# Optimization experiments

Hardware: AMD Instinct MI355X
Metric: run time of the kernel (lower is better)

Reference implementation:

```python
import jax, jax.numpy as jnp
import numpy as np

INV_SQRT2 = 0.7071067811865476
INV_SQRT3 = 0.5773502691896258

N_ATOMS, N_EDGES = 5000, 50000
K3, K4 = 16, 16
N_TRIP, N_QUAD = N_EDGES * K3, N_EDGES * K4
N_INTERM = N_QUAD // 2
NSPH3, NSPH4 = 7, 16
E_ATOM, E_EDGE = 128, 512
E_TRIP, E_QUAD = 64, 64
E_RBF, E_CBF, E_SBF = 16, 16, 32
E_BIL_T, E_BIL_Q = 64, 32


def _w(key, shape):
    # He-style init, fan_in = second-to-last dim
    return jax.random.normal(key, shape, jnp.float32) / np.float32(np.sqrt(shape[-2]))


def setup_inputs() -> dict:
    ks = iter(jax.random.split(jax.random.key(0), 64))
    nk = lambda: next(ks)
    inp = {}
    inp['h'] = jax.random.normal(nk(), (N_ATOMS, E_ATOM), jnp.float32)
    inp['m'] = jax.random.normal(nk(), (N_EDGES, E_EDGE), jnp.float32)
    inp['rbf4'] = jax.random.normal(nk(), (N_EDGES, E_RBF), jnp.float32)
    inp['cbf4'] = jax.random.normal(nk(), (N_INTERM, E_CBF), jnp.float32)
    inp['rbf_W1_4'] = jax.random.normal(nk(), (N_EDGES, E_SBF, NSPH4), jnp.float32) * 0.1
    inp['sph4'] = jax.random.normal(nk(), (N_EDGES, K4, NSPH4), jnp.float32) * 0.1
    inp['rbf3'] = jax.random.normal(nk(), (N_EDGES, E_RBF), jnp.float32)
    inp['rbf_W1_3'] = jax.random.normal(nk(), (N_EDGES, E_CBF, NSPH3), jnp.float32) * 0.1
    inp['sph3'] = jax.random.normal(nk(), (N_EDGES, K3, NSPH3), jnp.float32) * 0.1
    inp['rbf_h'] = jax.random.normal(nk(), (N_EDGES, E_RBF), jnp.float32)
    # learned parameters
    inp['W_dense_ca'] = _w(nk(), (E_EDGE, E_EDGE))
    inp['Wq_db'] = _w(nk(), (E_EDGE, E_EDGE))
    inp['Wq_rbf'] = _w(nk(), (E_RBF, E_EDGE))
    inp['Wq_cbf'] = _w(nk(), (E_CBF, E_QUAD))
    inp['Wq_bil'] = jax.random.normal(nk(), (E_QUAD, E_SBF, E_BIL_Q), jnp.float32) / np.float32(np.sqrt(E_QUAD * E_SBF))
    inp['Wq_down'] = _w(nk(), (E_EDGE, E_QUAD))
    inp['Wq_up_ca'] = _w(nk(), (E_BIL_Q, E_EDGE))
    inp['Wq_up_ac'] = _w(nk(), (E_BIL_Q, E_EDGE))
    inp['Wt_ba'] = _w(nk(), (E_EDGE, E_EDGE))
    inp['Wt_rbf'] = _w(nk(), (E_RBF, E_EDGE))
    inp['Wt_bil'] = jax.random.normal(nk(), (E_TRIP, E_CBF, E_BIL_T), jnp.float32) / np.float32(np.sqrt(E_TRIP * E_CBF))
    inp['Wt_down'] = _w(nk(), (E_EDGE, E_TRIP))
    inp['Wt_up_ca'] = _w(nk(), (E_BIL_T, E_EDGE))
    inp['Wt_up_ac'] = _w(nk(), (E_BIL_T, E_EDGE))
    inp['W_before'] = _w(nk(), (1, 2, E_EDGE, E_EDGE))
    inp['W_after'] = _w(nk(), (2, 2, E_EDGE, E_EDGE))
    inp['W_au_rbf'] = _w(nk(), (E_RBF, E_EDGE))
    inp['W_au_dense'] = _w(nk(), (E_EDGE, E_ATOM))
    inp['W_au_res'] = _w(nk(), (3, 2, E_ATOM, E_ATOM))
    inp['W_concat'] = _w(nk(), (2 * E_ATOM + E_EDGE, E_EDGE))
    inp['W_resm'] = _w(nk(), (1, 2, E_EDGE, E_EDGE))
    # index tensors; (id_reduce, Kidx) pairs are collision-free by construction
    i32 = jnp.int32
    inp['Kidx4'] = jnp.tile(jnp.arange(K4, dtype=i32), N_EDGES)
    inp['id_swap'] = jax.random.permutation(nk(), N_EDGES).astype(i32)
    inp['id4_reduce_ca'] = jnp.repeat(jnp.arange(N_EDGES, dtype=i32), K4)
    inp['id4_expand_intm_db'] = jax.random.randint(nk(), (N_INTERM,), 0, N_EDGES, i32)
    inp['id4_expand_abd'] = jax.random.randint(nk(), (N_QUAD,), 0, N_INTERM, i32)
    inp['Kidx3'] = jnp.tile(jnp.arange(K3, dtype=i32), N_EDGES)
    inp['id3_expand_ba'] = jax.random.randint(nk(), (N_TRIP,), 0, N_EDGES, i32)
    inp['id3_reduce_ca'] = jnp.repeat(jnp.arange(N_EDGES, dtype=i32), K3)
    inp['idx_s'] = jax.random.randint(nk(), (N_EDGES,), 0, N_ATOMS, i32)
    inp['idx_t'] = jax.random.randint(nk(), (N_EDGES,), 0, N_ATOMS, i32)
    return inp


def _residual_stack(x, Ws):
    # Ws: (L, 2, U, U); GemNet ResidualLayer: (x + f(f(x))) / sqrt(2)
    for i in range(Ws.shape[0]):
        y = jax.nn.silu(jax.nn.silu(x @ Ws[i, 0]) @ Ws[i, 1])
        x = (x + y) * INV_SQRT2
    return x


def _bilinear(rbf_W1, sph, mvals, W, id_reduce, Kidx):
    # EfficientInteractionBilinear: scatter interactions into (nEdges, Kmax, emb),
    # contract with spherical basis, down-projected radial basis and bilinear weight.
    nE, Kmax = sph.shape[0], sph.shape[1]
    m2 = jnp.zeros((nE, Kmax, mvals.shape[-1]), mvals.dtype).at[id_reduce, Kidx].set(mvals)
    sum_k = jnp.einsum('ekn,ekh->enh', sph, m2)    # (nEdges, nSph, emb)
    r = jnp.einsum('ein,enh->eih', rbf_W1, sum_k)  # (nEdges, interm, emb)
    return jnp.einsum('eih,hiu->eu', r, W)         # (nEdges, units_out)


def reference(h, m, rbf4, cbf4, rbf_W1_4, sph4, rbf3, rbf_W1_3, sph3, rbf_h,
              W_dense_ca, Wq_db, Wq_rbf, Wq_cbf, Wq_bil, Wq_down, Wq_up_ca, Wq_up_ac,
              Wt_ba, Wt_rbf, Wt_bil, Wt_down, Wt_up_ca, Wt_up_ac,
              W_before, W_after, W_au_rbf, W_au_dense, W_au_res, W_concat, W_resm,
              Kidx4, id_swap, id4_reduce_ca, id4_expand_intm_db, id4_expand_abd,
              Kidx3, id3_expand_ba, id3_reduce_ca, idx_s, idx_t):
    silu = jax.nn.silu
    x_ca_skip = silu(m @ W_dense_ca)
    # ---- quadruplet interaction ----
    xq = silu(m @ Wq_db)
    xq = xq * (rbf4 @ Wq_rbf)        # Hadamard with RBF (ScalingFactor scale=1)
    xq = silu(xq @ Wq_down)          # (nEdges, E_QUAD)
    xq = xq[id4_expand_intm_db]      # (nInterm, E_QUAD)
    xq = xq * (cbf4 @ Wq_cbf)        # Hadamard with CBF
    xq = xq[id4_expand_abd]          # (nQuad, E_QUAD)
    xq = _bilinear(rbf_W1_4, sph4, xq, Wq_bil, id4_reduce_ca, Kidx4)
    x4 = (silu(xq @ Wq_up_ca) + silu(xq @ Wq_up_ac)[id_swap]) * INV_SQRT2
    # ---- triplet interaction ----
    xt = silu(m @ Wt_ba)
    xt = xt * (rbf3 @ Wt_rbf)
    xt = silu(xt @ Wt_down)          # (nEdges, E_TRIP)
    xt = xt[id3_expand_ba]           # (nTrip, E_TRIP)
    xt = _bilinear(rbf_W1_3, sph3, xt, Wt_bil, id3_reduce_ca, Kidx3)
    x3 = (silu(xt @ Wt_up_ca) + silu(xt @ Wt_up_ac)[id_swap]) * INV_SQRT2
    # ---- merge + residual stacks ----
    x = (x_ca_skip + x3 + x4) * INV_SQRT3
    x = _residual_stack(x, W_before)
    m = (m + x) * INV_SQRT2
    m = _residual_stack(m, W_after)
    # ---- atom update ----
    xa = m * (rbf_h @ W_au_rbf)
    xa = jax.ops.segment_sum(xa, idx_t, num_segments=h.shape[0])
    xa = silu(xa @ W_au_dense)
    xa = _residual_stack(xa, W_au_res)
    h = (h + xa) * INV_SQRT2
    # ---- concat / edge re-embedding ----
    m2 = jnp.concatenate([h[idx_s], h[idx_t], m], axis=-1)
    m2 = silu(m2 @ W_concat)
    m2 = _residual_stack(m2, W_resm)
    m = (m + m2) * INV_SQRT2
    return h, m
```

## Files before the change

### kernel.cpp

```cpp
#include <hip/hip_runtime.h>

#define INV_SQRT2f 0.70710678118654752440f
#define INV_SQRT3f 0.57735026918962576451f

typedef __bf16 bf16x8 __attribute__((ext_vector_type(8)));
typedef float f32x4 __attribute__((ext_vector_type(4)));

__device__ __forceinline__ float silu_f(float x) { return x / (1.0f + __expf(-x)); }

enum { EPI_SILU = 0, EPI_SILU_MUL = 1, EPI_ACC = 2, EPI_RES = 3, EPI_RES2 = 4, EPI_NONE = 5 };

struct WT { const float* src; __bf16* dst; int K; int N; };
struct WTBatch { WT d[18]; };

__global__ __launch_bounds__(256) void wconv_k(WTBatch b)
{
  __shared__ float t[64][65];
  const WT w = b.d[blockIdx.z];
  const int k0 = blockIdx.x << 6, n0 = blockIdx.y << 6;
  if (k0 >= w.K || n0 >= w.N) return;
  const int tx = threadIdx.x & 63, ty = threadIdx.x >> 6;
#pragma unroll
  for (int i = 0; i < 16; ++i) {
    const int k = (i << 2) + ty;
    const int gk = k0 + k, gn = n0 + tx;
    t[k][tx] = (gk < w.K && gn < w.N) ? w.src[(size_t)gk * w.N + gn] : 0.0f;
  }
  __syncthreads();
#pragma unroll
  for (int i = 0; i < 16; ++i) {
    const int n = (i << 2) + ty;
    const int gn = n0 + n, gk = k0 + tx;
    if (gn < w.N && gk < w.K) w.dst[(size_t)gn * w.K + gk] = (__bf16)t[tx][n];
  }
}

template <int EPI, bool CONCAT, bool ABF16 = false>
__global__ __launch_bounds__(256) void gemm_k(
    const float* A, const __bf16* W, float* C, int M, int N, int K,
    const float* mul, const int* perm, const float* res0, const float* res1,
    float scale, const float* h_src, const int* gidx_s, const int* gidx_t,
    const float* m_src)
{
  constexpr int LSTR = 40;
  __shared__ __bf16 As[128 * LSTR];
  __shared__ __bf16 Bs[128 * LSTR];
  const int tid  = threadIdx.x;
  const int lane = tid & 63;
  const int wave = tid >> 6;
  const int bm = blockIdx.x << 7;
  const int bn = blockIdx.y << 7;
  const int wm = (wave & 1) << 6;
  const int wn = (wave >> 1) << 6;
  const int fm = lane & 15;
  const int qk = (lane >> 4) << 3;

  f32x4 acc[4][4] = {};

  const int nkt = K >> 5;
  for (int kt = 0; kt < nkt; ++kt) {
    const int k0 = kt << 5;
    if constexpr (ABF16) {
      const __bf16* Ab = (const __bf16*)A;
#pragma unroll
      for (int i = 0; i < 2; ++i) {
        const int f   = tid + (i << 8);
        const int row = f >> 2;
        const int c8  = (f & 3) << 3;
        int gm = bm + row;
        if (gm >= M) gm = M - 1;
        const bf16x8 v = *(const bf16x8*)(Ab + (size_t)gm * K + k0 + c8);
        *(bf16x8*)&As[row * LSTR + c8] = v;
      }
    } else {
#pragma unroll
      for (int i = 0; i < 4; ++i) {
        const int f   = tid + (i << 8);
        const int row = f >> 3;
        const int c4  = (f & 7) << 2;
        int gm = bm + row;
        if (gm >= M) gm = M - 1;
        const int gk = k0 + c4;
        float4 v;
        if (CONCAT) {
          const float* src;
          if (gk < 128)      src = h_src + ((size_t)gidx_s[gm] << 7) + gk;
          else if (gk < 256) src = h_src + ((size_t)gidx_t[gm] << 7) + (gk - 128);
          else               src = m_src + ((size_t)gm << 9) + (gk - 256);
          v = *(const float4*)src;
        } else {
          v = *(const float4*)(A + (size_t)gm * K + gk);
        }
        __bf16* dst = &As[row * LSTR + c4];
        dst[0] = (__bf16)v.x; dst[1] = (__bf16)v.y;
        dst[2] = (__bf16)v.z; dst[3] = (__bf16)v.w;
      }
    }
#pragma unroll
    for (int i = 0; i < 2; ++i) {
      const int f  = tid + (i << 8);
      const int n  = f >> 2;
      const int c8 = (f & 3) << 3;
      int gn = bn + n;
      if (gn >= N) gn = N - 1;
      const bf16x8 v = *(const bf16x8*)(W + (size_t)gn * K + k0 + c8);
      *(bf16x8*)&Bs[n * LSTR + c8] = v;
    }
    __syncthreads();
    bf16x8 af[4], bfv[4];
#pragma unroll
    for (int mt = 0; mt < 4; ++mt)
      af[mt] = *(const bf16x8*)&As[(wm + mt * 16 + fm) * LSTR + qk];
#pragma unroll
    for (int nt = 0; nt < 4; ++nt)
      bfv[nt] = *(const bf16x8*)&Bs[(wn + nt * 16 + fm) * LSTR + qk];
#pragma unroll
    for (int mt = 0; mt < 4; ++mt)
#pragma unroll
      for (int nt = 0; nt < 4; ++nt)
        acc[mt][nt] = __builtin_amdgcn_mfma_f32_16x16x32_bf16(af[mt], bfv[nt], acc[mt][nt], 0, 0, 0);
    __syncthreads();
  }

#pragma unroll
  for (int mt = 0; mt < 4; ++mt) {
#pragma unroll
    for (int nt = 0; nt < 4; ++nt) {
#pragma unroll
      for (int r = 0; r < 4; ++r) {
        const int row = bm + wm + mt * 16 + ((lane >> 4) << 2) + r;
        const int col = bn + wn + nt * 16 + fm;
        if (row < M && col < N) {
          const float s = acc[mt][nt][r];
          const size_t o = (size_t)row * N + col;
          if constexpr (EPI == EPI_SILU) {
            C[o] = silu_f(s) * scale;
          } else if constexpr (EPI == EPI_SILU_MUL) {
            C[o] = silu_f(s) * mul[o];
          } else if constexpr (EPI == EPI_ACC) {
            const int rr = perm ? perm[row] : row;
            C[(size_t)rr * N + col] += silu_f(s) * scale;
          } else if constexpr (EPI == EPI_RES) {
            C[o] = (res0[o] + silu_f(s)) * scale;
          } else if constexpr (EPI == EPI_RES2) {
            C[o] = (res0[o] + (res1[o] + silu_f(s)) * INV_SQRT2f) * INV_SQRT2f;
          } else {
            C[o] = s * scale;
          }
        }
      }
    }
  }
}

__global__ __launch_bounds__(256) void rbf_proj_k(
    const float* __restrict__ rbf, const float* __restrict__ W,
    float* __restrict__ out, int M)
{
  const int g = blockIdx.x * 256 + threadIdx.x;
  const int e = g >> 9, c = g & 511;
  if (e >= M) return;
  const float* r = rbf + (size_t)e * 16;
  float s = 0.0f;
#pragma unroll
  for (int j = 0; j < 16; ++j) s += r[j] * W[(j << 9) + c];
  out[g] = s;
}

__global__ __launch_bounds__(256) void quad_interm_k(
    const float* __restrict__ xqe, const float* __restrict__ cbf,
    const float* __restrict__ Wcbf, const int* __restrict__ idb,
    float* __restrict__ out)
{
  __shared__ float Ws[1024];
  const int t = threadIdx.x;
  for (int i = t; i < 1024; i += 256) Ws[i] = Wcbf[i];
  __syncthreads();
  const int i = blockIdx.x * 4 + (t >> 6);
  const int c = t & 63;
  const float* cb = cbf + (size_t)i * 16;
  float s = 0.0f;
#pragma unroll
  for (int j = 0; j < 16; ++j) s += cb[j] * Ws[j * 64 + c];
  out[(size_t)i * 64 + c] = xqe[(size_t)idb[i] * 64 + c] * s;
}

__global__ __launch_bounds__(256) void quad_r_k(
    const float* __restrict__ BI, const float* __restrict__ sph,
    const float* __restrict__ rbfW, const int* __restrict__ abd,
    __bf16* __restrict__ R)
{
  __shared__ float sp[4][256];
  __shared__ float rw[4][512];
  const int t = threadIdx.x;
  const int lane = t & 63;
  const int w = t >> 6;
  const int e = blockIdx.x * 4 + w;

  *(float4*)&sp[w][lane << 2] = *(const float4*)(sph + (size_t)e * 256 + (lane << 2));
  *(float4*)&rw[w][lane << 2] = *(const float4*)(rbfW + (size_t)e * 512 + (lane << 2));
  *(float4*)&rw[w][256 + (lane << 2)] = *(const float4*)(rbfW + (size_t)e * 512 + 256 + (lane << 2));

  float val[16];
#pragma unroll
  for (int k = 0; k < 16; ++k)
    val[k] = BI[(size_t)abd[e * 16 + k] * 64 + lane];

  __syncthreads();

  float sumk[16] = {};
#pragma unroll
  for (int k = 0; k < 16; ++k) {
    const float v = val[k];
#pragma unroll
    for (int n = 0; n < 16; ++n) sumk[n] += sp[w][k * 16 + n] * v;
  }

#pragma unroll
  for (int ib = 0; ib < 4; ++ib) {
    bf16x8 pack;
#pragma unroll
    for (int j = 0; j < 8; ++j) {
      const int i = ib * 8 + j;
      float s = 0.0f;
#pragma unroll
      for (int n = 0; n < 16; ++n) s += rw[w][i * 16 + n] * sumk[n];
      pack[j] = (__bf16)s;
    }
    *(bf16x8*)(R + (size_t)e * 2048 + (lane << 5) + (ib << 3)) = pack;
  }
}

__global__ __launch_bounds__(256) void trip_r_k(
    const float* __restrict__ XTE, const float* __restrict__ sph,
    const float* __restrict__ rbfW, const int* __restrict__ ba,
    __bf16* __restrict__ R)
{
  __shared__ float sp[4][112];
  __shared__ float rw[4][112];
  const int t = threadIdx.x;
  const int lane = t & 63;
  const int w = t >> 6;
  const int e = blockIdx.x * 4 + w;

  if (lane < 28) {
    *(float4*)&sp[w][lane << 2] = *(const float4*)(sph + (size_t)e * 112 + (lane << 2));
  } else if (lane >= 32 && lane < 60) {
    const int q = (lane - 32) << 2;
    *(float4*)&rw[w][q] = *(const float4*)(rbfW + (size_t)e * 112 + q);
  }

  float val[16];
#pragma unroll
  for (int k = 0; k < 16; ++k)
    val[k] = XTE[(size_t)ba[e * 16 + k] * 64 + lane];

  __syncthreads();

  float sumk[7] = {};
#pragma unroll
  for (int k = 0; k < 16; ++k) {
    const float v = val[k];
#pragma unroll
    for (int n = 0; n < 7; ++n) sumk[n] += sp[w][k * 7 + n] * v;
  }

#pragma unroll
  for (int ib = 0; ib < 2; ++ib) {
    bf16x8 pack;
#pragma unroll
    for (int j = 0; j < 8; ++j) {
      const int i = ib * 8 + j;
      float s = 0.0f;
#pragma unroll
      for (int n = 0; n < 7; ++n) s += rw[w][i * 7 + n] * sumk[n];
      pack[j] = (__bf16)s;
    }
    *(bf16x8*)(R + (size_t)e * 1024 + (lane << 4) + (ib << 3)) = pack;
  }
}

__global__ __launch_bounds__(256) void inv_perm_k(const int* __restrict__ p,
                                                  int* __restrict__ inv, int n)
{
  const int i = blockIdx.x * 256 + threadIdx.x;
  if (i < n) inv[p[i]] = i;
}

__global__ __launch_bounds__(256) void zero_k(float* __restrict__ p, int n)
{
  const int i = blockIdx.x * 256 + threadIdx.x;
  if (i < n) p[i] = 0.0f;
}

__global__ __launch_bounds__(256) void atom_scatter_k(
    const float* __restrict__ mafter, const float* __restrict__ rh,
    const int* __restrict__ idxt, float* __restrict__ A0, int nE)
{
  const int g = blockIdx.x * 256 + threadIdx.x;
  const int e = g >> 9, c = g & 511;
  if (e >= nE) return;
  const size_t o = (size_t)e * 512 + c;
  atomicAdd(&A0[(size_t)idxt[e] * 512 + c], mafter[o] * rh[o]);
}

__global__ __launch_bounds__(256) void hout_k(const float* __restrict__ h,
                                              const float* __restrict__ xa,
                                              float* __restrict__ out, int n)
{
  const int i = blockIdx.x * 256 + threadIdx.x;
  if (i < n) out[i] = (h[i] + xa[i]) * INV_SQRT2f;
}

extern "C" void kernel_launch(void* const* d_in, const int* in_sizes, int n_in,
                              void* d_out, int out_size, void* d_ws, size_t ws_size,
                              hipStream_t stream) {
  (void)in_sizes; (void)n_in; (void)out_size; (void)ws_size;
  const float* h        = (const float*)d_in[0];
  const float* m        = (const float*)d_in[1];
  const float* rbf4     = (const float*)d_in[2];
  const float* cbf4     = (const float*)d_in[3];
  const float* rbfW4    = (const float*)d_in[4];
  const float* sph4     = (const float*)d_in[5];
  const float* rbf3     = (const float*)d_in[6];
  const float* rbfW3    = (const float*)d_in[7];
  const float* sph3     = (const float*)d_in[8];
  const float* rbf_h    = (const float*)d_in[9];
  const float* W_dense  = (const float*)d_in[10];
  const float* Wq_db    = (const float*)d_in[11];
  const float* Wq_rbf   = (const float*)d_in[12];
  const float* Wq_cbf   = (const float*)d_in[13];
  const float* Wq_bil   = (const float*)d_in[14];
  const float* Wq_down  = (const float*)d_in[15];
  const float* Wq_up_ca = (const float*)d_in[16];
  const float* Wq_up_ac = (const float*)d_in[17];
  const float* Wt_ba    = (const float*)d_in[18];
  const float* Wt_rbf   = (const float*)d_in[19];
  const float* Wt_bil   = (const float*)d_in[20];
  const float* Wt_down  = (const float*)d_in[21];
  const float* Wt_up_ca = (const float*)d_in[22];
  const float* Wt_up_ac = (const float*)d_in[23];
  const float* W_before = (const float*)d_in[24];
  const float* W_after  = (const float*)d_in[25];
  const float* W_au_rbf = (const float*)d_in[26];
  const float* W_au_dns = (const float*)d_in[27];
  const float* W_au_res = (const float*)d_in[28];
  const float* W_concat = (const float*)d_in[29];
  const float* W_resm   = (const float*)d_in[30];
  const int* id_swap    = (const int*)d_in[32];
  const int* id4_db     = (const int*)d_in[34];
  const int* id4_abd    = (const int*)d_in[35];
  const int* id3_ba     = (const int*)d_in[37];
  const int* idx_s      = (const int*)d_in[39];
  const int* idx_t      = (const int*)d_in[40];

  float* w = (float*)d_ws;
  const size_t S = 25600000;
  float* B0  = w;
  float* B1  = w + S;
  float* XQE = B1;
  float* XTE = B1;
  __bf16* RQ = (__bf16*)w;
  __bf16* RT = (__bf16*)w;
  float* R   = w + 2 * S;
  float* XQB = R;
  float* XTB = R + 1600000;
  float* A0  = R;
  float* A1  = R + 2560000;
  float* A2  = R + 3200000;
  int*   INV = (int*)(R + 4800000);

  float* out_h = (float*)d_out;
  float* out_m = out_h + 640000;
  float* BI    = out_m;

  WTBatch b1{}, b2{}, b3{};
  int n1 = 0, n2 = 0, n3 = 0;
  __bf16* z1p = (__bf16*)out_h;
  __bf16* z5p = (__bf16*)(R + 3840000);
  __bf16* z3p = (__bf16*)R;
  auto cv1 = [&](const float* s, int K, int N) { __bf16* d = z1p; z1p += (size_t)K * N; b1.d[n1++] = WT{s, d, K, N}; return d; };
  auto cv2 = [&](const float* s, int K, int N) { __bf16* d = z5p; z5p += (size_t)K * N; b2.d[n2++] = WT{s, d, K, N}; return d; };
  auto cv3 = [&](const float* s, int K, int N) { __bf16* d = z3p; z3p += (size_t)K * N; b3.d[n3++] = WT{s, d, K, N}; return d; };

  __bf16* Wb_q_db    = cv1(Wq_db,    512, 512);
  __bf16* Wb_q_down  = cv1(Wq_down,  512,  64);
  __bf16* Wb_q_bil   = cv1(Wq_bil,  2048,  32);
  __bf16* Wb_t_ba    = cv1(Wt_ba,    512, 512);
  __bf16* Wb_t_down  = cv1(Wt_down,  512,  64);
  __bf16* Wb_t_bil   = cv1(Wt_bil,  1024,  64);
  __bf16* Wb_dense   = cv1(W_dense,  512, 512);
  __bf16* Wb_q_up_ca = cv1(Wq_up_ca,  32, 512);
  __bf16* Wb_q_up_ac = cv1(Wq_up_ac,  32, 512);
  __bf16* Wb_t_up_ca = cv1(Wt_up_ca,  64, 512);
  __bf16* Wb_t_up_ac = cv1(Wt_up_ac,  64, 512);
  __bf16* Wb_au_dns  = cv1(W_au_dns, 512, 128);
  __bf16* Wb_au_res[6];
  for (int l = 0; l < 6; ++l) Wb_au_res[l] = cv1(W_au_res + (size_t)l * 16384, 128, 128);
  __bf16* Wb_before0 = cv2(W_before,          512, 512);
  __bf16* Wb_before1 = cv2(W_before + 262144, 512, 512);
  __bf16* Wb_after[4];
  for (int l = 0; l < 4; ++l) Wb_after[l] = cv2(W_after + (size_t)l * 262144, 512, 512);
  __bf16* Wb_concat  = cv3(W_concat,        768, 512);
  __bf16* Wb_resm0   = cv3(W_resm,          512, 512);
  __bf16* Wb_resm1   = cv3(W_resm + 262144, 512, 512);

  const float s23 = INV_SQRT2f * INV_SQRT3f;
  const dim3 blk(256);
  const dim3 gFull(391, 4), gN64(391, 1), gBil(391, 1), gAtom(40, 1);
#define NUL9 nullptr, nullptr, nullptr, nullptr
#define TAIL4 nullptr, nullptr, nullptr, nullptr

  wconv_k<<<dim3(32, 8, n1), blk, 0, stream>>>(b1);
  inv_perm_k<<<196, blk, 0, stream>>>(id_swap, INV, 50000);

  rbf_proj_k<<<100000, blk, 0, stream>>>(rbf4, Wq_rbf, B1, 50000);
  gemm_k<EPI_SILU_MUL, false><<<gFull, blk, 0, stream>>>(m, Wb_q_db, B0, 50000, 512, 512,
      B1, nullptr, nullptr, nullptr, 1.0f, TAIL4);
  gemm_k<EPI_SILU, false><<<gN64, blk, 0, stream>>>(B0, Wb_q_down, XQE, 50000, 64, 512,
      NUL9, 1.0f, TAIL4);
  quad_interm_k<<<100000, blk, 0, stream>>>(XQE, cbf4, Wq_cbf, id4_db, BI);
  quad_r_k<<<12500, blk, 0, stream>>>(BI, sph4, rbfW4, id4_abd, RQ);
  gemm_k<EPI_NONE, false, true><<<gBil, blk, 0, stream>>>((const float*)RQ, Wb_q_bil, XQB,
      50000, 32, 2048, NUL9, 1.0f, TAIL4);

  rbf_proj_k<<<100000, blk, 0, stream>>>(rbf3, Wt_rbf, B1, 50000);
  gemm_k<EPI_SILU_MUL, false><<<gFull, blk, 0, stream>>>(m, Wb_t_ba, B0, 50000, 512, 512,
      B1, nullptr, nullptr, nullptr, 1.0f, TAIL4);
  gemm_k<EPI_SILU, false><<<gN64, blk, 0, stream>>>(B0, Wb_t_down, XTE, 50000, 64, 512,
      NUL9, 1.0f, TAIL4);
  trip_r_k<<<12500, blk, 0, stream>>>(XTE, sph3, rbfW3, id3_ba, RT);
  gemm_k<EPI_NONE, false, true><<<gBil, blk, 0, stream>>>((const float*)RT, Wb_t_bil, XTB,
      50000, 64, 1024, NUL9, 1.0f, TAIL4);

  gemm_k<EPI_SILU, false><<<gFull, blk, 0, stream>>>(m, Wb_dense, B0, 50000, 512, 512,
      NUL9, INV_SQRT3f, TAIL4);
  gemm_k<EPI_ACC, false><<<gFull, blk, 0, stream>>>(XQB, Wb_q_up_ca, B0, 50000, 512, 32,
      nullptr, nullptr, nullptr, nullptr, s23, TAIL4);
  gemm_k<EPI_ACC, false><<<gFull, blk, 0, stream>>>(XQB, Wb_q_up_ac, B0, 50000, 512, 32,
      nullptr, INV, nullptr, nullptr, s23, TAIL4);
  gemm_k<EPI_ACC, false><<<gFull, blk, 0, stream>>>(XTB, Wb_t_up_ca, B0, 50000, 512, 64,
      nullptr, nullptr, nullptr, nullptr, s23, TAIL4);
  gemm_k<EPI_ACC, false><<<gFull, blk, 0, stream>>>(XTB, Wb_t_up_ac, B0, 50000, 512, 64,
      nullptr, INV, nullptr, nullptr, s23, TAIL4);

  wconv_k<<<dim3(8, 8, n2), blk, 0, stream>>>(b2);

  gemm_k<EPI_SILU, false><<<gFull, blk, 0, stream>>>(B0, Wb_before0, B1, 50000, 512, 512,
      NUL9, 1.0f, TAIL4);
  gemm_k<EPI_RES2, false><<<gFull, blk, 0, stream>>>(B1, Wb_before1, out_m, 50000, 512, 512,
      nullptr, nullptr, m, B0, 1.0f, TAIL4);
  gemm_k<EPI_SILU, false><<<gFull, blk, 0, stream>>>(out_m, Wb_after[0], B1, 50000, 512, 512,
      NUL9, 1.0f, TAIL4);
  gemm_k<EPI_RES, false><<<gFull, blk, 0, stream>>>(B1, Wb_after[1], out_m, 50000, 512, 512,
      nullptr, nullptr, out_m, nullptr, INV_SQRT2f, TAIL4);
  gemm_k<EPI_SILU, false><<<gFull, blk, 0, stream>>>(out_m, Wb_after[2], B1, 50000, 512, 512,
      NUL9, 1.0f, TAIL4);
  gemm_k<EPI_RES, false><<<gFull, blk, 0, stream>>>(B1, Wb_after[3], out_m, 50000, 512, 512,
      nullptr, nullptr, out_m, nullptr, INV_SQRT2f, TAIL4);

  rbf_proj_k<<<100000, blk, 0, stream>>>(rbf_h, W_au_rbf, B1, 50000);
  zero_k<<<10000, blk, 0, stream>>>(A0, 2560000);
  atom_scatter_k<<<100000, blk, 0, stream>>>(out_m, B1, idx_t, A0, 50000);
  gemm_k<EPI_SILU, false><<<gAtom, blk, 0, stream>>>(A0, Wb_au_dns, A1, 5000, 128, 512,
      NUL9, 1.0f, TAIL4);
  for (int l = 0; l < 3; ++l) {
    gemm_k<EPI_SILU, false><<<gAtom, blk, 0, stream>>>(A1, Wb_au_res[2 * l],
        A2, 5000, 128, 128, NUL9, 1.0f, TAIL4);
    gemm_k<EPI_RES, false><<<gAtom, blk, 0, stream>>>(A2, Wb_au_res[2 * l + 1],
        A1, 5000, 128, 128, nullptr, nullptr, A1, nullptr, INV_SQRT2f, TAIL4);
  }
  hout_k<<<2500, blk, 0, stream>>>(h, A1, out_h, 640000);

  wconv_k<<<dim3(12, 8, n3), blk, 0, stream>>>(b3);

  gemm_k<EPI_SILU, true><<<gFull, blk, 0, stream>>>(nullptr, Wb_concat, B0, 50000, 512, 768,
      nullptr, nullptr, nullptr, nullptr, 1.0f, out_h, idx_s, idx_t, out_m);
  gemm_k<EPI_SILU, false><<<gFull, blk, 0, stream>>>(B0, Wb_resm0, B1, 50000, 512, 512,
      NUL9, 1.0f, TAIL4);
  gemm_k<EPI_RES2, false><<<gFull, blk, 0, stream>>>(B1, Wb_resm1, out_m, 50000, 512, 512,
      nullptr, nullptr, out_m, B0, 1.0f, TAIL4);
#undef NUL9
#undef TAIL4
}
```

Baseline: 3.202 ms.

## Use bf16 intermediates, direct-to-LDS async loads, and register prefetch of A tiles

GEMMs whose outputs feed only another GEMM now write bf16 instead of fp32, and the consuming GEMMs read bf16 A operands. Weight and bf16 A tiles are loaded straight from global memory into LDS with global_load_lds 16-byte transfers using an unpadded stride. The fp32 A path prefetches the next k-tile into registers while the current tile is being multiplied. The aim is to cut intermediate memory traffic and hide load latency, in exchange for bf16 rounding of intermediates and possible LDS bank conflicts from dropping the padding.

```diff
diff --git a/kernel.cpp b/kernel.cpp
--- a/kernel.cpp
+++ b/kernel.cpp
@@ -8,7 +8,11 @@
 
 __device__ __forceinline__ float silu_f(float x) { return x / (1.0f + __expf(-x)); }
 
-enum { EPI_SILU = 0, EPI_SILU_MUL = 1, EPI_ACC = 2, EPI_RES = 3, EPI_RES2 = 4, EPI_NONE = 5 };
+enum { EPI_SILU = 0, EPI_SILU_MUL = 1, EPI_ACC = 2, EPI_RES = 3, EPI_RES2 = 4, EPI_NONE = 5, EPI_SILU2 = 6 };
+
+#define GLD16(gp, lp) __builtin_amdgcn_global_load_lds( \
+    (const __attribute__((address_space(1))) void*)(gp), \
+    (__attribute__((address_space(3))) void*)(lp), 16, 0, 0)
 
 struct WT { const float* src; __bf16* dst; int K; int N; };
 struct WTBatch { WT d[18]; };
@@ -35,16 +39,16 @@
   }
 }
 
-template <int EPI, bool CONCAT, bool ABF16 = false>
+template <int EPI, bool CONCAT, bool ABF16 = false, bool OBF16 = false>
 __global__ __launch_bounds__(256) void gemm_k(
     const float* A, const __bf16* W, float* C, int M, int N, int K,
     const float* mul, const int* perm, const float* res0, const float* res1,
     float scale, const float* h_src, const int* gidx_s, const int* gidx_t,
     const float* m_src)
 {
-  constexpr int LSTR = 40;
-  __shared__ __bf16 As[128 * LSTR];
-  __shared__ __bf16 Bs[128 * LSTR];
+  constexpr int ASTR = ABF16 ? 32 : 40;
+  __shared__ __bf16 As[128 * ASTR];
+  __shared__ __bf16 Bs[128 * 32];
   const int tid  = threadIdx.x;
   const int lane = tid & 63;
   const int wave = tid >> 6;
@@ -54,23 +58,47 @@
   const int wn = (wave >> 1) << 6;
   const int fm = lane & 15;
   const int qk = (lane >> 4) << 3;
+  const int r4 = lane >> 2;
+  const int c8 = (lane & 3) << 3;
 
   f32x4 acc[4][4] = {};
-
+  float4 apre[4];
+
+  const __bf16* Ab = (const __bf16*)A;
   const int nkt = K >> 5;
+
+  auto load_a = [&](int k0) {
+#pragma unroll
+    for (int i = 0; i < 4; ++i) {
+      const int f   = tid + (i << 8);
+      const int row = f >> 3;
+      const int c4  = (f & 7) << 2;
+      int gm = bm + row;
+      if (gm >= M) gm = M - 1;
+      const int gk = k0 + c4;
+      if (CONCAT) {
+        const float* src;
+        if (gk < 128)      src = h_src + ((size_t)gidx_s[gm] << 7) + gk;
+        else if (gk < 256) src = h_src + ((size_t)gidx_t[gm] << 7) + (gk - 128);
+        else               src = m_src + ((size_t)gm << 9) + (gk - 256);
+        apre[i] = *(const float4*)src;
+      } else {
+        apre[i] = *(const float4*)(A + (size_t)gm * K + gk);
+      }
+    }
+  };
+
+  if constexpr (!ABF16) load_a(0);
+
   for (int kt = 0; kt < nkt; ++kt) {
     const int k0 = kt << 5;
     if constexpr (ABF16) {
-      const __bf16* Ab = (const __bf16*)A;
 #pragma unroll
       for (int i = 0; i < 2; ++i) {
-        const int f   = tid + (i << 8);
-        const int row = f >> 2;
-        const int c8  = (f & 3) << 3;
-        int gm = bm + row;
+        const int rb = (wave << 5) + (i << 4);
+        int gm = bm + rb + r4;
         if (gm >= M) gm = M - 1;
-        const bf16x8 v = *(const bf16x8*)(Ab + (size_t)gm * K + k0 + c8);
-        *(bf16x8*)&As[row * LSTR + c8] = v;
+        GLD16(Ab + (size_t)gm * K + k0 + c8, &As[rb << 5]);
       }
     } else {
 #pragma unroll
@@ -78,42 +106,29 @@
         const int f   = tid + (i << 8);
         const int row = f >> 3;
         const int c4  = (f & 7) << 2;
-        int gm = bm + row;
-        if (gm >= M) gm = M - 1;
-        const int gk = k0 + c4;
-        float4 v;
-        if (CONCAT) {
-          const float* src;
-          if (gk < 128)      src = h_src + ((size_t)gidx_s[gm] << 7) + gk;
-          else if (gk < 256) src = h_src + ((size_t)gidx_t[gm] << 7) + (gk - 128);
-          else               src = m_src + ((size_t)gm << 9) + (gk - 256);
-          v = *(const float4*)src;
-        } else {
-          v = *(const float4*)(A + (size_t)gm * K + gk);
-        }
-        __bf16* dst = &As[row * LSTR + c4];
-        dst[0] = (__bf16)v.x; dst[1] = (__bf16)v.y;
-        dst[2] = (__bf16)v.z; dst[3] = (__bf16)v.w;
+        __bf16* dst = &As[row * ASTR + c4];
+        dst[0] = (__bf16)apre[i].x; dst[1] = (__bf16)apre[i].y;
+        dst[2] = (__bf16)apre[i].z; dst[3] = (__bf16)apre[i].w;
       }
     }
 #pragma unroll
     for (int i = 0; i < 2; ++i) {
-      const int f  = tid + (i << 8);
-      const int n  = f >> 2;
-      const int c8 = (f & 3) << 3;
-      int gn = bn + n;
+      const int rb = (wave << 5) + (i << 4);
+      int gn = bn + rb + r4;
       if (gn >= N) gn = N - 1;
-      const bf16x8 v = *(const bf16x8*)(W + (size_t)gn * K + k0 + c8);
-      *(bf16x8*)&Bs[n * LSTR + c8] = v;
+      GLD16(W + (size_t)gn * K + k0 + c8, &Bs[rb << 5]);
     }
     __syncthreads();
+    if constexpr (!ABF16) {
+      if (kt + 1 < nkt) load_a(k0 + 32);
+    }
     bf16x8 af[4], bfv[4];
 #pragma unroll
     for (int mt = 0; mt < 4; ++mt)
-      af[mt] = *(const bf16x8*)&As[(wm + mt * 16 + fm) * LSTR + qk];
+      af[mt] = *(const bf16x8*)&As[(wm + mt * 16 + fm) * ASTR + qk];
 #pragma unroll
     for (int nt = 0; nt < 4; ++nt)
-      bfv[nt] = *(const bf16x8*)&Bs[(wn + nt * 16 + fm) * LSTR + qk];
+      bfv[nt] = *(const bf16x8*)&Bs[((wn + nt * 16 + fm) << 5) + qk];
 #pragma unroll
     for (int mt = 0; mt < 4; ++mt)
 #pragma unroll
@@ -122,6 +137,8 @@
     __syncthreads();
   }
 
+  __bf16* Cb  = (__bf16*)C;
+  __bf16* C2b = (__bf16*)res0;
 #pragma unroll
   for (int mt = 0; mt < 4; ++mt) {
 #pragma unroll
@@ -134,9 +151,11 @@
           const float s = acc[mt][nt][r];
           const size_t o = (size_t)row * N + col;
           if constexpr (EPI == EPI_SILU) {
-            C[o] = silu_f(s) * scale;
+            const float v = silu_f(s) * scale;
+            if constexpr (OBF16) Cb[o] = (__bf16)v; else C[o] = v;
           } else if constexpr (EPI == EPI_SILU_MUL) {
-            C[o] = silu_f(s) * mul[o];
+            const float v = silu_f(s) * mul[o];
+            if constexpr (OBF16) Cb[o] = (__bf16)v; else C[o] = v;
           } else if constexpr (EPI == EPI_ACC) {
             const int rr = perm ? perm[row] : row;
             C[(size_t)rr * N + col] += silu_f(s) * scale;
@@ -144,6 +163,9 @@
             C[o] = (res0[o] + silu_f(s)) * scale;
           } else if constexpr (EPI == EPI_RES2) {
             C[o] = (res0[o] + (res1[o] + silu_f(s)) * INV_SQRT2f) * INV_SQRT2f;
+          } else if constexpr (EPI == EPI_SILU2) {
+            const float v = silu_f(s) * scale;
+            C[o] = v; C2b[o] = (__bf16)v;
           } else {
             C[o] = s * scale;
           }
@@ -370,6 +392,11 @@
   float* A2  = R + 3200000;
   int*   INV = (int*)(R + 4800000);
 
+  __bf16* B0b  = (__bf16*)B0;
+  __bf16* B1b  = (__bf16*)B1;
+  __bf16* CCb  = (__bf16*)B1;
+  __bf16* RMb  = (__bf16*)(B1 + 12800000);
+
   float* out_h = (float*)d_out;
   float* out_m = out_h + 640000;
   float* BI    = out_m;
@@ -415,20 +442,20 @@
   inv_perm_k<<<196, blk, 0, stream>>>(id_swap, INV, 50000);
 
   rbf_proj_k<<<100000, blk, 0, stream>>>(rbf4, Wq_rbf, B1, 50000);
-  gemm_k<EPI_SILU_MUL, false><<<gFull, blk, 0, stream>>>(m, Wb_q_db, B0, 50000, 512, 512,
-      B1, nullptr, nullptr, nullptr, 1.0f, TAIL4);
-  gemm_k<EPI_SILU, false><<<gN64, blk, 0, stream>>>(B0, Wb_q_down, XQE, 50000, 64, 512,
-      NUL9, 1.0f, TAIL4);
+  gemm_k<EPI_SILU_MUL, false, false, true><<<gFull, blk, 0, stream>>>(m, Wb_q_db, B0,
+      50000, 512, 512, B1, nullptr, nullptr, nullptr, 1.0f, TAIL4);
+  gemm_k<EPI_SILU, false, true><<<gN64, blk, 0, stream>>>((const float*)B0b, Wb_q_down, XQE,
+      50000, 64, 512, NUL9, 1.0f, TAIL4);
   quad_interm_k<<<100000, blk, 0, stream>>>(XQE, cbf4, Wq_cbf, id4_db, BI);
   quad_r_k<<<12500, blk, 0, stream>>>(BI, sph4, rbfW4, id4_abd, RQ);
   gemm_k<EPI_NONE, false, true><<<gBil, blk, 0, stream>>>((const float*)RQ, Wb_q_bil, XQB,
       50000, 32, 2048, NUL9, 1.0f, TAIL4);
 
   rbf_proj_k<<<100000, blk, 0, stream>>>(rbf3, Wt_rbf, B1, 50000);
-  gemm_k<EPI_SILU_MUL, false><<<gFull, blk, 0, stream>>>(m, Wb_t_ba, B0, 50000, 512, 512,
-      B1, nullptr, nullptr, nullptr, 1.0f, TAIL4);
-  gemm_k<EPI_SILU, false><<<gN64, blk, 0, stream>>>(B0, Wb_t_down, XTE, 50000, 64, 512,
-      NUL9, 1.0f, TAIL4);
+  gemm_k<EPI_SILU_MUL, false, false, true><<<gFull, blk, 0, stream>>>(m, Wb_t_ba, B0,
+      50000, 512, 512, B1, nullptr, nullptr, nullptr, 1.0f, TAIL4);
+  gemm_k<EPI_SILU, false, true><<<gN64, blk, 0, stream>>>((const float*)B0b, Wb_t_down, XTE,
+      50000, 64, 512, NUL9, 1.0f, TAIL4);
   trip_r_k<<<12500, blk, 0, stream>>>(XTE, sph3, rbfW3, id3_ba, RT);
   gemm_k<EPI_NONE, false, true><<<gBil, blk, 0, stream>>>((const float*)RT, Wb_t_bil, XTB,
       50000, 64, 1024, NUL9, 1.0f, TAIL4);
@@ -446,18 +473,18 @@
 
   wconv_k<<<dim3(8, 8, n2), blk, 0, stream>>>(b2);
 
-  gemm_k<EPI_SILU, false><<<gFull, blk, 0, stream>>>(B0, Wb_before0, B1, 50000, 512, 512,
-      NUL9, 1.0f, TAIL4);
-  gemm_k<EPI_RES2, false><<<gFull, blk, 0, stream>>>(B1, Wb_before1, out_m, 50000, 512, 512,
-      nullptr, nullptr, m, B0, 1.0f, TAIL4);
-  gemm_k<EPI_SILU, false><<<gFull, blk, 0, stream>>>(out_m, Wb_after[0], B1, 50000, 512, 512,
-      NUL9, 1.0f, TAIL4);
-  gemm_k<EPI_RES, false><<<gFull, blk, 0, stream>>>(B1, Wb_after[1], out_m, 50000, 512, 512,
-      nullptr, nullptr, out_m, nullptr, INV_SQRT2f, TAIL4);
-  gemm_k<EPI_SILU, false><<<gFull, blk, 0, stream>>>(out_m, Wb_after[2], B1, 50000, 512, 512,
-      NUL9, 1.0f, TAIL4);
-  gemm_k<EPI_RES, false><<<gFull, blk, 0, stream>>>(B1, Wb_after[3], out_m, 50000, 512, 512,
-      nullptr, nullptr, out_m, nullptr, INV_SQRT2f, TAIL4);
+  gemm_k<EPI_SILU, false, false, true><<<gFull, blk, 0, stream>>>(B0, Wb_before0, B1,
+      50000, 512, 512, NUL9, 1.0f, TAIL4);
+  gemm_k<EPI_RES2, false, true><<<gFull, blk, 0, stream>>>((const float*)B1b, Wb_before1, out_m,
+      50000, 512, 512, nullptr, nullptr, m, B0, 1.0f, TAIL4);
+  gemm_k<EPI_SILU, false, false, true><<<gFull, blk, 0, stream>>>(out_m, Wb_after[0], B1,
+      50000, 512, 512, NUL9, 1.0f, TAIL4);
+  gemm_k<EPI_RES, false, true><<<gFull, blk, 0, stream>>>((const float*)B1b, Wb_after[1], out_m,
+      50000, 512, 512, nullptr, nullptr, out_m, nullptr, INV_SQRT2f, TAIL4);
+  gemm_k<EPI_SILU, false, false, true><<<gFull, blk, 0, stream>>>(out_m, Wb_after[2], B1,
+      50000, 512, 512, NUL9, 1.0f, TAIL4);
+  gemm_k<EPI_RES, false, true><<<gFull, blk, 0, stream>>>((const float*)B1b, Wb_after[3], out_m,
+      50000, 512, 512, nullptr, nullptr, out_m, nullptr, INV_SQRT2f, TAIL4);
 
   rbf_proj_k<<<100000, blk, 0, stream>>>(rbf_h, W_au_rbf, B1, 50000);
   zero_k<<<10000, blk, 0, stream>>>(A0, 2560000);
@@ -474,12 +501,13 @@
 
   wconv_k<<<dim3(12, 8, n3), blk, 0, stream>>>(b3);
 
-  gemm_k<EPI_SILU, true><<<gFull, blk, 0, stream>>>(nullptr, Wb_concat, B0, 50000, 512, 768,
-      nullptr, nullptr, nullptr, nullptr, 1.0f, out_h, idx_s, idx_t, out_m);
-  gemm_k<EPI_SILU, false><<<gFull, blk, 0, stream>>>(B0, Wb_resm0, B1, 50000, 512, 512,
-      NUL9, 1.0f, TAIL4);
-  gemm_k<EPI_RES2, false><<<gFull, blk, 0, stream>>>(B1, Wb_resm1, out_m, 50000, 512, 512,
-      nullptr, nullptr, out_m, B0, 1.0f, TAIL4);
+  gemm_k<EPI_SILU2, true><<<gFull, blk, 0, stream>>>(nullptr, Wb_concat, B0,
+      50000, 512, 768, nullptr, nullptr, (const float*)CCb, nullptr, 1.0f,
+      out_h, idx_s, idx_t, out_m);
+  gemm_k<EPI_SILU, false, true, true><<<gFull, blk, 0, stream>>>((const float*)CCb, Wb_resm0,
+      (float*)RMb, 50000, 512, 512, NUL9, 1.0f, TAIL4);
+  gemm_k<EPI_RES2, false, true><<<gFull, blk, 0, stream>>>((const float*)RMb, Wb_resm1, out_m,
+      50000, 512, 512, nullptr, nullptr, out_m, B0, 1.0f, TAIL4);
 #undef NUL9
 #undef TAIL4
 }
```

New measurement: 3.297 ms. 1.03x slower.
